# Performance work log

Measured on AMD Instinct MI355X. Metric: run time of the kernel, lower is better.

Reference implementation:

```python
import jax, jax.numpy as jnp
import numpy as np

MIN_RANGE, MAX_RANGE = 1, 3

def _build_offsets():
    # replicates TorchGrouper.__init__: offsets over a hollow cube neighborhood
    r = np.concatenate([np.arange(-MAX_RANGE, -MIN_RANGE), np.arange(MIN_RANGE, MAX_RANGE)])
    p = r.shape[0]
    rx = np.broadcast_to(r.reshape(1, 1, -1), (p, p, p))
    ry = np.broadcast_to(r.reshape(1, -1, 1), (p, p, p))
    rz = np.broadcast_to(r.reshape(-1, 1, 1), (p, p, p))
    off = np.stack([np.zeros_like(rx), rx, ry, rz], axis=3).reshape(-1, 4)  # [O,4], cols (0,x,y,z)
    return jnp.asarray(off, dtype=jnp.int32)


def setup_inputs() -> dict:
    key = jax.random.key(0)
    k1, k2, k3, k4 = jax.random.split(key, 4)
    N, Z, Y, X = 2, 40, 400, 400
    G, M, C = 40000, 100000, 64
    # voxel map values in [-1, M-1]; -1 == empty voxel (maps to zero feature row)
    voxel_maps = jax.random.randint(k1, (N, Z, Y, X), -1, M, dtype=jnp.int32)
    b = jax.random.randint(k2, (G, 1), 0, N).astype(jnp.float32)
    zyx = jax.random.uniform(k3, (G, 3), dtype=jnp.float32) * jnp.array([Z - 1, Y - 1, X - 1], jnp.float32)
    grid_positions = jnp.concatenate([b, zyx], axis=1)  # [G,4] float (batch,z,y,x)
    features = jax.random.normal(k4, (M, C), dtype=jnp.float32)
    return {"voxel_maps": voxel_maps, "grid_positions": grid_positions, "features": features}


def reference(voxel_maps, grid_positions, features):
    offsets = _build_offsets()                     # [O,4] int32
    O = offsets.shape[0]
    N, Z, Y, X = voxel_maps.shape
    G = grid_positions.shape[0]

    gp_f = grid_positions[:, None, :] + offsets[None].astype(grid_positions.dtype)  # [G,O,4] float
    gp = gp_f.astype(jnp.int32)                    # trunc-toward-zero, matches torch .long()
    bi = gp[..., 0]
    zi = jnp.clip(gp[..., 1], 0, Z - 1)
    yi = jnp.clip(gp[..., 2], 0, Y - 1)
    xi = jnp.clip(gp[..., 3], 0, X - 1)
    sampled_idx = voxel_maps[bi, zi, yi, xi]       # [G,O] int32

    feats_pad = jnp.concatenate([jnp.zeros((1, features.shape[1]), features.dtype), features], axis=0)  # [M+1,C]
    sf = feats_pad[sampled_idx + 1]                # [G,O,C]
    sampled_features = jnp.transpose(sf, (2, 0, 1))[None]  # [1,C,G,O]

    gpf = jnp.transpose(gp_f[..., 1:], (2, 0, 1))[None]    # [1,3,G,O] (z,y,x) coords
    gpf = gpf - jnp.trunc(gpf)                     # fractional part (torch .long().float())
    # faithful quirk: original adds index_offset[:, :3] == columns (0, x, y)
    gpf = gpf + offsets[:, :3].T.astype(gpf.dtype).reshape(1, 3, 1, O)

    empty_mask = jnp.sum(sampled_idx + 1, axis=1) == 0     # [G] bool
    return sampled_features, gpf, empty_mask
```

## Files before the change

### kernel.cpp

```cpp
#include <hip/hip_runtime.h>


constexpr int G  = 40000;
constexpr int O  = 64;
constexpr int C  = 64;
constexpr int VZ = 40, VY = 400, VX = 400;
constexpr long long GO = (long long)G * O;

__global__ __launch_bounds__(256) void grouper_kernel(
    const int*   __restrict__ vox,
    const float* __restrict__ gpos,
    const float* __restrict__ feat,
    float*       __restrict__ out)
{
    const int tid = blockIdx.x * 256 + threadIdx.x;
    const int g = tid >> 6;
    const int o = tid & 63;

    const int rtab4[4] = {-3, -2, 1, 2};
    const int rx = rtab4[o & 3];
    const int ry = rtab4[(o >> 2) & 3];
    const int rz = rtab4[(o >> 4) & 3];

    const float4 p = ((const float4*)gpos)[g];
    const float zf = p.y + (float)rx;
    const float yf = p.z + (float)ry;
    const float xf = p.w + (float)rz;

    const int bi = (int)p.x;
    const int zi = min(max((int)zf, 0), VZ - 1);
    const int yi = min(max((int)yf, 0), VY - 1);
    const int xi = min(max((int)xf, 0), VX - 1);

    const int idx = vox[((bi * VZ + zi) * VY + yi) * VX + xi];

    float* gout = out + (size_t)C * GO;
    __builtin_nontemporal_store(zf - truncf(zf),               gout + tid);
    __builtin_nontemporal_store(yf - truncf(yf) + (float)rx,   gout + GO + tid);
    __builtin_nontemporal_store(xf - truncf(xf) + (float)ry,   gout + 2 * GO + tid);

    const int allm1 = __all(idx == -1);
    if (o == 0) gout[3 * GO + g] = allm1 ? 1.0f : 0.0f;

    const bool empty = (idx < 0);
    const int row = empty ? 0 : idx;
    const float4* frow = (const float4*)(feat + (size_t)row * C);
    float* op = out + tid;
    #pragma unroll
    for (int c4 = 0; c4 < C / 4; ++c4) {
        float4 v = frow[c4];
        v.x = empty ? 0.0f : v.x;
        v.y = empty ? 0.0f : v.y;
        v.z = empty ? 0.0f : v.z;
        v.w = empty ? 0.0f : v.w;
        __builtin_nontemporal_store(v.x, op + (size_t)(4 * c4 + 0) * GO);
        __builtin_nontemporal_store(v.y, op + (size_t)(4 * c4 + 1) * GO);
        __builtin_nontemporal_store(v.z, op + (size_t)(4 * c4 + 2) * GO);
        __builtin_nontemporal_store(v.w, op + (size_t)(4 * c4 + 3) * GO);
    }
}

extern "C" void kernel_launch(void* const* d_in, const int* in_sizes, int n_in,
                              void* d_out, int out_size, void* d_ws, size_t ws_size,
                              hipStream_t stream) {
    const int*   vox  = (const int*)d_in[0];
    const float* gpos = (const float*)d_in[1];
    const float* feat = (const float*)d_in[2];
    float*       out  = (float*)d_out;

    const int total = (int)GO;
    const int block = 256;
    const int grid  = (total + block - 1) / block;
    grouper_kernel<<<grid, block, 0, stream>>>(vox, gpos, feat, out);
}
```

Measured before the change: 200.3 us.

## Transpose gathered feature rows through swizzled LDS for coalesced vector stores

Each wavefront now handles one grid point. Lanes cooperatively gather feature rows as contiguous 16-byte vectors, with eight lanes per row. The rows are staged in a per-wave LDS tile using an XOR swizzle, then read back transposed so each lane writes a float4 of four consecutive offsets for one channel. This replaces the uncoalesced per-thread 256-byte row reads and the scalar channel-major stores with fully coalesced gather reads and vectorized stores. The cost is 32KB of LDS per block, which may limit occupancy, and it relies on wave-local ordering with waitcnt instead of a barrier.

```diff
diff --git a/kernel.cpp b/kernel.cpp
--- a/kernel.cpp
+++ b/kernel.cpp
@@ -1,11 +1,12 @@
 #include <hip/hip_runtime.h>
 
 
+typedef float f32x4 __attribute__((ext_vector_type(4)));
+
 constexpr int G  = 40000;
-constexpr int O  = 64;
 constexpr int C  = 64;
 constexpr int VZ = 40, VY = 400, VX = 400;
-constexpr long long GO = (long long)G * O;
+constexpr size_t GO = (size_t)G * 64;
 
 __global__ __launch_bounds__(256) void grouper_kernel(
     const int*   __restrict__ vox,
@@ -13,9 +14,12 @@
     const float* __restrict__ feat,
     float*       __restrict__ out)
 {
-    const int tid = blockIdx.x * 256 + threadIdx.x;
-    const int g = tid >> 6;
-    const int o = tid & 63;
+    __shared__ __align__(16) float lds[4][64 * 32];
+
+    const int wid  = threadIdx.x >> 6;
+    const int lane = threadIdx.x & 63;
+    const int g = blockIdx.x * 4 + wid;
+    const int o = lane;
 
     const int rtab4[4] = {-3, -2, 1, 2};
     const int rx = rtab4[o & 3];
@@ -34,29 +38,47 @@
 
     const int idx = vox[((bi * VZ + zi) * VY + yi) * VX + xi];
 
-    float* gout = out + (size_t)C * GO;
-    __builtin_nontemporal_store(zf - truncf(zf),               gout + tid);
-    __builtin_nontemporal_store(yf - truncf(yf) + (float)rx,   gout + GO + tid);
-    __builtin_nontemporal_store(xf - truncf(xf) + (float)ry,   gout + 2 * GO + tid);
-
+    float* gout = out + C * GO;
+    const size_t t = (size_t)g * 64 + o;
+    __builtin_nontemporal_store(zf - truncf(zf),             gout + t);
+    __builtin_nontemporal_store(yf - truncf(yf) + (float)rx, gout + GO + t);
+    __builtin_nontemporal_store(xf - truncf(xf) + (float)ry, gout + 2 * GO + t);
     const int allm1 = __all(idx == -1);
     if (o == 0) gout[3 * GO + g] = allm1 ? 1.0f : 0.0f;
 
-    const bool empty = (idx < 0);
-    const int row = empty ? 0 : idx;
-    const float4* frow = (const float4*)(feat + (size_t)row * C);
-    float* op = out + tid;
+    float* tile = lds[wid];
+    const int d  = lane >> 3;
+    const int c4 = lane & 7;
+    const int q  = lane >> 4;
+    const int m  = lane & 15;
+
     #pragma unroll
-    for (int c4 = 0; c4 < C / 4; ++c4) {
-        float4 v = frow[c4];
-        v.x = empty ? 0.0f : v.x;
-        v.y = empty ? 0.0f : v.y;
-        v.z = empty ? 0.0f : v.z;
-        v.w = empty ? 0.0f : v.w;
-        __builtin_nontemporal_store(v.x, op + (size_t)(4 * c4 + 0) * GO);
-        __builtin_nontemporal_store(v.y, op + (size_t)(4 * c4 + 1) * GO);
-        __builtin_nontemporal_store(v.z, op + (size_t)(4 * c4 + 2) * GO);
-        __builtin_nontemporal_store(v.w, op + (size_t)(4 * c4 + 3) * GO);
+    for (int chunk = 0; chunk < 2; ++chunk) {
+        #pragma unroll
+        for (int i = 0; i < 8; ++i) {
+            const int r    = i * 8 + d;
+            const int ridx = __shfl(idx, r);
+            const bool emp = ridx < 0;
+            const int  rr  = emp ? 0 : ridx;
+            f32x4 v = *(const f32x4*)(feat + (size_t)rr * C + chunk * 32 + c4 * 4);
+            if (emp) { v.x = 0.0f; v.y = 0.0f; v.z = 0.0f; v.w = 0.0f; }
+            const int cs = c4 ^ ((r >> 2) & 7);
+            *(f32x4*)(tile + r * 32 + cs * 4) = v;
+        }
+        asm volatile("s_waitcnt lgkmcnt(0)" ::: "memory");
+
+        #pragma unroll
+        for (int i = 0; i < 8; ++i) {
+            const int ip = (i ^ (m & 7)) * 4 + q;
+            f32x4 sv;
+            sv.x = tile[(m * 4 + 0) * 32 + ip];
+            sv.y = tile[(m * 4 + 1) * 32 + ip];
+            sv.z = tile[(m * 4 + 2) * 32 + ip];
+            sv.w = tile[(m * 4 + 3) * 32 + ip];
+            const size_t c = (size_t)(chunk * 32 + i * 4 + q);
+            __builtin_nontemporal_store(sv, (f32x4*)(out + c * GO + (size_t)g * 64 + m * 4));
+        }
+        asm volatile("s_waitcnt lgkmcnt(0)" ::: "memory");
     }
 }
 
@@ -68,8 +90,6 @@
     const float* feat = (const float*)d_in[2];
     float*       out  = (float*)d_out;
 
-    const int total = (int)GO;
-    const int block = 256;
-    const int grid  = (total + block - 1) / block;
-    grouper_kernel<<<grid, block, 0, stream>>>(vox, gpos, feat, out);
+    const int grid = G / 4;
+    grouper_kernel<<<grid, 256, 0, stream>>>(vox, gpos, feat, out);
 }
```

Measured after the change: 200.0 us. No clear change (-0.1%).
